# Kernel optimization log

Hardware: AMD Instinct MI355X
Metric: run time of the kernel (lower is better)

The kernel has to match this reference:

```python
import jax, jax.numpy as jnp
import numpy as np

# SAWB clip coefficients (statistics-aware weight binning): alpha = C1*sqrt(E[w^2]) + C2*E[|w|]
SAWB_C1 = 12.68
SAWB_C2 = -12.80
Q_LEVELS = 127.0  # symmetric 8-bit


def sawb_quantize_sparse(W, mask):
    """Quantize only the nonzero (masked) weight values per-tensor, SAWB clip.
    Returns dequantized sparse weight (zeros stay zero), matching the
    original module which stores nnz values + indices and quantizes the
    nnz value vector."""
    m = mask.astype(W.dtype)
    n = jnp.maximum(jnp.sum(m), 1.0)
    m1 = jnp.sum(jnp.abs(W) * m) / n          # E[|w|] over nonzeros
    m2 = jnp.sum((W * W) * m) / n             # E[w^2] over nonzeros
    alpha = SAWB_C1 * jnp.sqrt(m2) + SAWB_C2 * m1
    scale = alpha / Q_LEVELS
    q = jnp.round(jnp.clip(W / scale, -Q_LEVELS, Q_LEVELS))
    return (q * scale) * m


def setup_inputs() -> dict:
    key = jax.random.key(0)
    k1, k2, k3, k4 = jax.random.split(key, 4)
    B, IC, H, Wsp = 16, 64, 224, 224
    OC, K = 64, 3
    x = jax.random.normal(k1, (B, IC, H, Wsp), dtype=jnp.float32)
    W = jax.random.normal(k2, (OC, IC, K, K), dtype=jnp.float32) * 0.05
    mask = jax.random.uniform(k3, (OC, IC, K, K)) > 0.9
    bias = jax.random.normal(k4, (OC,), dtype=jnp.float32) * 0.01
    return {"x": x, "W": W, "mask": mask, "bias": bias}


def reference(x, W, mask, bias):
    # Dequantized sparse weight (equivalent math to gather-based sparse
    # quantized conv kernel with fused dequant)
    Wq = sawb_quantize_sparse(W, mask)
    y = jax.lax.conv_general_dilated(
        x, Wq,
        window_strides=(1, 1),
        padding=((1, 1), (1, 1)),
        dimension_numbers=("NCHW", "OIHW", "NCHW"),
    )
    return y + bias[None, :, None, None]
```

## Files before the change

### kernel.cpp

```cpp
#include <hip/hip_runtime.h>
#include <hip/hip_bf16.h>
#include <math.h>

typedef __bf16 bfx8 __attribute__((ext_vector_type(8)));
typedef float f32x4 __attribute__((ext_vector_type(4)));

#define NELEM_W 36864
#define CHW     50176

__device__ __forceinline__ int detect_mask_kind(const void* mask, int tid, int nthreads,
                                                int* s_flags, int* s_kind) {
  if (tid < 8) s_flags[tid] = 0;
  __syncthreads();
  const unsigned int* mw = (const unsigned int*)mask;
  int lowbf = 0, notf32 = 0, anyf32 = 0, noti32 = 0, anyi1 = 0;
  for (int i = tid; i < 1024; i += nthreads) {
    unsigned v = mw[i];
    if ((v & 0xFFFFu) == 0x3F80u) lowbf = 1;
    if (!(v == 0u || v == 0x3F800000u)) notf32 = 1;
    if (v == 0x3F800000u) anyf32 = 1;
    if (!(v == 0u || v == 1u)) noti32 = 1;
    if (v == 1u) anyi1 = 1;
  }
  if (lowbf)  atomicOr(&s_flags[0], 1);
  if (notf32) atomicOr(&s_flags[1], 1);
  if (anyf32) atomicOr(&s_flags[2], 1);
  if (noti32) atomicOr(&s_flags[3], 1);
  if (anyi1)  atomicOr(&s_flags[4], 1);
  __syncthreads();
  if (tid == 0) {
    int kind;
    if (s_flags[0]) kind = 3;
    else if (!s_flags[1] && s_flags[2]) kind = 2;
    else if (!s_flags[3] && s_flags[4]) kind = 1;
    else kind = 0;
    *s_kind = kind;
  }
  __syncthreads();
  return *s_kind;
}

__device__ __forceinline__ bool mask_val(const void* mask, int kind, int e) {
  switch (kind) {
    case 1:  return ((const int*)mask)[e] != 0;
    case 2:  return ((const float*)mask)[e] != 0.0f;
    case 3:  return ((const unsigned short*)mask)[e] != 0;
    default: return ((const unsigned char*)mask)[e] != 0;
  }
}

__global__ __launch_bounds__(512) void stats_kernel(const float* __restrict__ W,
                                                    const void* __restrict__ mask,
                                                    float* __restrict__ ws_part) {
  __shared__ int s_flags[8]; __shared__ int s_kind;
  __shared__ float s_red[3][8];
  const int tid = threadIdx.x;
  int kind = detect_mask_kind(mask, tid, 512, s_flags, &s_kind);
  int e = blockIdx.x * 512 + tid;
  float w = W[e];
  bool m = mask_val(mask, kind, e);
  float s1 = m ? fabsf(w) : 0.f;
  float s2 = m ? w * w   : 0.f;
  float c  = m ? 1.f     : 0.f;
  #pragma unroll
  for (int o = 32; o > 0; o >>= 1) {
    s1 += __shfl_down(s1, o); s2 += __shfl_down(s2, o); c += __shfl_down(c, o);
  }
  int wv = tid >> 6;
  if ((tid & 63) == 0) { s_red[0][wv] = s1; s_red[1][wv] = s2; s_red[2][wv] = c; }
  __syncthreads();
  if (tid == 0) {
    float a = 0, b = 0, cc = 0;
    for (int i = 0; i < 8; i++) { a += s_red[0][i]; b += s_red[1][i]; cc += s_red[2][i]; }
    ws_part[blockIdx.x * 4 + 0] = a;
    ws_part[blockIdx.x * 4 + 1] = b;
    ws_part[blockIdx.x * 4 + 2] = cc;
  }
}

__global__ __launch_bounds__(512) void quant_kernel(const float* __restrict__ W,
                                                    const void* __restrict__ mask,
                                                    const float* __restrict__ ws_part,
                                                    float* __restrict__ ws_scale,
                                                    unsigned short* __restrict__ Bq) {
  __shared__ int s_flags[8]; __shared__ int s_kind;
  __shared__ float s_scale;
  const int tid = threadIdx.x;
  int kind = detect_mask_kind(mask, tid, 512, s_flags, &s_kind);
  if (tid == 0) {
    float a = 0, b = 0, cc = 0;
    for (int i = 0; i < 72; i++) { a += ws_part[i*4]; b += ws_part[i*4+1]; cc += ws_part[i*4+2]; }
    float n  = fmaxf(cc, 1.f);
    float m1 = a / n, m2 = b / n;
    float alpha = 12.68f * sqrtf(m2) - 12.80f * m1;
    float scale = alpha / 127.0f;
    s_scale = scale;
    if (blockIdx.x == 0) ws_scale[0] = scale;
  }
  __syncthreads();
  float scale = s_scale;
  int e = blockIdx.x * 512 + tid;
  float w = W[e];
  float q = 0.f;
  if (mask_val(mask, kind, e)) {
    float v = w / scale;
    v = fminf(fmaxf(v, -127.f), 127.f);
    q = rintf(v);
  }
  int kxy = e % 9; int t = e / 9; int ic = t & 63; int oc = t >> 6;
  __bf16 qb = (__bf16)q;
  Bq[(kxy * 64 + oc) * 64 + ic] = *(unsigned short*)&qb;
}

__global__ __launch_bounds__(512, 6) void conv_kernel(const float* __restrict__ x,
    const unsigned short* __restrict__ Bq, const float* __restrict__ ws_scale,
    const float* __restrict__ bias, float* __restrict__ out)
{
  __shared__ __align__(16) unsigned char smem[6 * 66 * 128];
  const int tid = threadIdx.x;

  int lin = blockIdx.x + (int)(gridDim.x * (blockIdx.y + gridDim.y * blockIdx.z));
  int logical = (lin & 7) * 448 + (lin >> 3);
  const int bx = logical & 3;
  int rr = logical >> 2;
  const int by = rr % 56;
  const int b  = rr / 56;
  const int x0 = bx * 64;
  const int y0 = by * 4;

  for (int e = tid; e < 6 * 8 * 66; e += 512) {
    int col = e % 66; int t = e / 66; int icg = t & 7; int row = t >> 3;
    int grow = y0 - 1 + row, gcol = x0 - 1 + col;
    bfx8 v;
    if ((unsigned)grow < 224u && (unsigned)gcol < 224u) {
      const float* src = x + (((size_t)(b * 64 + icg * 8)) * 224 + grow) * 224 + gcol;
      #pragma unroll
      for (int j = 0; j < 8; j++) v[j] = (__bf16)src[j * CHW];
    } else {
      #pragma unroll
      for (int j = 0; j < 8; j++) v[j] = (__bf16)0.f;
    }
    int off = ((row * 66 + col) * 128 + icg * 16) ^ ((col & 7) << 4);
    *(bfx8*)(smem + off) = v;
  }
  __syncthreads();

  const int w = tid >> 6, lane = tid & 63;
  const int l15 = lane & 15, lg = lane >> 4;
  const int wrow = w >> 1;
  const int oc0  = (w & 1) * 32;

  f32x4 acc[4][2];
  #pragma unroll
  for (int m = 0; m < 4; m++) { acc[m][0] = {0.f,0.f,0.f,0.f}; acc[m][1] = {0.f,0.f,0.f,0.f}; }

  #pragma unroll
  for (int ky = 0; ky < 3; ky++) {
    const int lrow = wrow + ky;
    #pragma unroll
    for (int kx = 0; kx < 3; kx++) {
      #pragma unroll
      for (int icb = 0; icb < 2; icb++) {
        const int ick = icb * 32 + lg * 8;
        const unsigned short* wp = Bq + (((ky*3 + kx) * 64 + oc0 + l15) * 64 + ick);
        bfx8 wf0 = *(const bfx8*)wp;
        bfx8 wf1 = *(const bfx8*)(wp + 16 * 64);
        #pragma unroll
        for (int m = 0; m < 4; m++) {
          int colw = kx + m * 16 + l15;
          int off  = ((lrow * 66 + colw) * 128 + ick * 2) ^ ((colw & 7) << 4);
          bfx8 xf  = *(const bfx8*)(smem + off);
          acc[m][0] = __builtin_amdgcn_mfma_f32_16x16x32_bf16(wf0, xf, acc[m][0], 0, 0, 0);
          acc[m][1] = __builtin_amdgcn_mfma_f32_16x16x32_bf16(wf1, xf, acc[m][1], 0, 0, 0);
        }
      }
    }
  }

  const float scale = ws_scale[0];
  const int yr = y0 + wrow;
  #pragma unroll
  for (int m = 0; m < 4; m++) {
    const int gcol = x0 + m * 16 + l15;
    if (gcol < 224) {
      #pragma unroll
      for (int n = 0; n < 2; n++) {
        #pragma unroll
        for (int r = 0; r < 4; r++) {
          int oc = oc0 + n * 16 + lg * 4 + r;
          out[(((size_t)(b * 64 + oc)) * 224 + yr) * 224 + gcol] = acc[m][n][r] * scale + bias[oc];
        }
      }
    }
  }
}

extern "C" void kernel_launch(void* const* d_in, const int* in_sizes, int n_in,
                              void* d_out, int out_size, void* d_ws, size_t ws_size,
                              hipStream_t stream) {
  const float* x    = (const float*)d_in[0];
  const float* W    = (const float*)d_in[1];
  const void*  mask = d_in[2];
  const float* bias = (const float*)d_in[3];
  float* out = (float*)d_out;

  float*          ws_part  = (float*)d_ws;
  float*          ws_scale = (float*)((char*)d_ws + 2048);
  unsigned short* Bq       = (unsigned short*)((char*)d_ws + 4096);

  stats_kernel<<<72, 512, 0, stream>>>(W, mask, ws_part);
  quant_kernel<<<72, 512, 0, stream>>>(W, mask, ws_part, ws_scale, Bq);
  dim3 grid(4, 56, 16);
  conv_kernel<<<grid, 512, 0, stream>>>(x, Bq, ws_scale, bias, out);
}
```

Measured before the change: 475.9 us.

## Prepack input to padded bf16 channel-last layout and use async LDS loads with 32x32 MFMA

Adds a prepass kernel that converts the fp32 NCHW input into a padded, swizzled bf16 channel-interleaved buffer in workspace. The conv kernel then fills its LDS halo tile with direct global-to-LDS async 16-byte copies instead of strided fp32 gathers and conversions. It also switches to 32x32x16 MFMA tiles. This costs an extra full pass over the input (read fp32, write bf16) plus a workspace size check with a fallback path.

```diff
diff --git a/kernel.cpp b/kernel.cpp
--- a/kernel.cpp
+++ b/kernel.cpp
@@ -4,9 +4,22 @@
 
 typedef __bf16 bfx8 __attribute__((ext_vector_type(8)));
 typedef float f32x4 __attribute__((ext_vector_type(4)));
+typedef float f32x16 __attribute__((ext_vector_type(16)));
+typedef unsigned short u16x8 __attribute__((ext_vector_type(8)));
 
 #define NELEM_W 36864
 #define CHW     50176
+#define XB_ROWPITCH 28928
+#define XB_BYTES (16*224*XB_ROWPITCH)
+#define ZP_OFF   81920
+#define XB_OFF   98304
+#define WS_NEED  ((size_t)XB_OFF + (size_t)XB_BYTES)
+
+__device__ __forceinline__ void async_cp16(const void* g, void* l) {
+  __builtin_amdgcn_global_load_lds(
+      (const __attribute__((address_space(1))) unsigned int*)g,
+      (__attribute__((address_space(3))) unsigned int*)l, 16, 0, 0);
+}
 
 __device__ __forceinline__ int detect_mask_kind(const void* mask, int tid, int nthreads,
                                                 int* s_flags, int* s_kind) {
@@ -82,7 +95,8 @@
                                                     const void* __restrict__ mask,
                                                     const float* __restrict__ ws_part,
                                                     float* __restrict__ ws_scale,
-                                                    unsigned short* __restrict__ Bq) {
+                                                    unsigned short* __restrict__ Bq,
+                                                    char* __restrict__ zp) {
   __shared__ int s_flags[8]; __shared__ int s_kind;
   __shared__ float s_scale;
   const int tid = threadIdx.x;
@@ -100,21 +114,64 @@
   __syncthreads();
   float scale = s_scale;
   int e = blockIdx.x * 512 + tid;
-  float w = W[e];
-  float q = 0.f;
-  if (mask_val(mask, kind, e)) {
-    float v = w / scale;
-    v = fminf(fmaxf(v, -127.f), 127.f);
-    q = rintf(v);
-  }
-  int kxy = e % 9; int t = e / 9; int ic = t & 63; int oc = t >> 6;
-  __bf16 qb = (__bf16)q;
-  Bq[(kxy * 64 + oc) * 64 + ic] = *(unsigned short*)&qb;
-}
-
-__global__ __launch_bounds__(512, 6) void conv_kernel(const float* __restrict__ x,
-    const unsigned short* __restrict__ Bq, const float* __restrict__ ws_scale,
-    const float* __restrict__ bias, float* __restrict__ out)
+  if (e < NELEM_W) {
+    float w = W[e];
+    float q = 0.f;
+    if (mask_val(mask, kind, e)) {
+      float v = w / scale;
+      v = fminf(fmaxf(v, -127.f), 127.f);
+      q = rintf(v);
+    }
+    int kxy = e % 9; int t = e / 9; int ic = t & 63; int oc = t >> 6;
+    __bf16 qb = (__bf16)q;
+    Bq[(kxy * 64 + oc) * 64 + ic] = *(unsigned short*)&qb;
+  } else {
+    f32x4 z = {0.f, 0.f, 0.f, 0.f};
+    for (int u = tid; u < 528; u += 512) *(f32x4*)(zp + u * 16) = z;
+  }
+}
+
+__global__ __launch_bounds__(256) void prepass_kernel(const float* __restrict__ x,
+                                                      char* __restrict__ xb) {
+  __shared__ unsigned short lt[64][65];
+  const int cg = blockIdx.x;
+  const int h  = blockIdx.y;
+  const int b  = blockIdx.z;
+  const int t  = threadIdx.x;
+  const int c0 = cg * 64;
+  const int ncols = (226 - c0) < 64 ? (226 - c0) : 64;
+
+  {
+    int colt = t & 63, icq = t >> 6;
+    if (colt < ncols) {
+      int gcol = c0 + colt - 1;
+      bool valid = (unsigned)gcol < 224u;
+      const float* src = x + ((size_t)(b * 64 + icq * 16) * 224 + h) * 224 + gcol;
+      #pragma unroll
+      for (int j = 0; j < 16; j++) {
+        float v = valid ? src[(size_t)j * CHW] : 0.f;
+        __bf16 bv = (__bf16)v;
+        lt[icq * 16 + j][colt] = *(unsigned short*)&bv;
+      }
+    }
+  }
+  __syncthreads();
+  size_t rowbase = ((size_t)(b * 224 + h)) * XB_ROWPITCH;
+  for (int u = t; u < ncols * 8; u += 256) {
+    int colt = u >> 3, icg = u & 7;
+    int c = c0 + colt;
+    u16x8 v;
+    #pragma unroll
+    for (int j = 0; j < 8; j++) v[j] = lt[icg * 8 + j][colt];
+    int off = (c * 128 + icg * 16) ^ ((c & 7) << 4);
+    *(u16x8*)(xb + rowbase + off) = v;
+  }
+}
+
+__global__ __launch_bounds__(512, 6) void conv_kernel(const char* __restrict__ xb,
+    const char* __restrict__ zp, const unsigned short* __restrict__ Bq,
+    const float* __restrict__ ws_scale, const float* __restrict__ bias,
+    float* __restrict__ out)
 {
   __shared__ __align__(16) unsigned char smem[6 * 66 * 128];
   const int tid = threadIdx.x;
@@ -128,6 +185,86 @@
   const int x0 = bx * 64;
   const int y0 = by * 4;
 
+  const int w = tid >> 6, lane = tid & 63;
+
+  {
+    const size_t winoff = (size_t)x0 * 128;
+    #pragma unroll
+    for (int j = w; j < 48; j += 8) {
+      int row = j >> 3, chunk = j & 7;
+      int grow = y0 - 1 + row;
+      const char* src = ((unsigned)grow < 224u)
+          ? xb + ((size_t)(b * 224 + grow)) * XB_ROWPITCH + winoff + chunk * 1024
+          : zp + chunk * 1024;
+      async_cp16(src + lane * 16, smem + row * 8448 + chunk * 1024);
+    }
+    if (tid < 96) {
+      int row = tid >> 4, u = tid & 15;
+      int grow = y0 - 1 + row;
+      const char* src = ((unsigned)grow < 224u)
+          ? xb + ((size_t)(b * 224 + grow)) * XB_ROWPITCH + winoff + 8192 + u * 16
+          : zp + 8192 + u * 16;
+      *(f32x4*)(smem + row * 8448 + 8192 + u * 16) = *(const f32x4*)src;
+    }
+  }
+  __syncthreads();
+
+  const int wrow = w >> 1;
+  const int ch   = w & 1;
+  const int l31  = lane & 31, lg2 = lane >> 5;
+
+  f32x16 acc0 = {}, acc1 = {};
+
+  #pragma unroll
+  for (int ky = 0; ky < 3; ky++) {
+    const int lrow = wrow + ky;
+    #pragma unroll
+    for (int kx = 0; kx < 3; kx++) {
+      const int kxy = ky * 3 + kx;
+      #pragma unroll
+      for (int icq = 0; icq < 4; icq++) {
+        const int ick = icq * 16 + lg2 * 8;
+        const int ct  = kx + ch * 32 + l31;
+        const int off = (lrow * 66 + ct) * 128 + ((ick * 2) ^ ((ct & 7) << 4));
+        bfx8 xf = *(const bfx8*)(smem + off);
+        const unsigned short* wp = Bq + ((kxy * 64 + l31) * 64 + ick);
+        bfx8 wf0 = *(const bfx8*)wp;
+        bfx8 wf1 = *(const bfx8*)(wp + 32 * 64);
+        acc0 = __builtin_amdgcn_mfma_f32_32x32x16_bf16(wf0, xf, acc0, 0, 0, 0);
+        acc1 = __builtin_amdgcn_mfma_f32_32x32x16_bf16(wf1, xf, acc1, 0, 0, 0);
+      }
+    }
+  }
+
+  const float scale = ws_scale[0];
+  const int yr = y0 + wrow;
+  const int gcol = x0 + ch * 32 + l31;
+  if (gcol < 224) {
+    #pragma unroll
+    for (int r = 0; r < 16; r++) {
+      int ocr = (r & 3) + 8 * (r >> 2) + 4 * lg2;
+      size_t o0 = (((size_t)(b * 64 + ocr)) * 224 + yr) * 224 + gcol;
+      out[o0]              = acc0[r] * scale + bias[ocr];
+      out[o0 + 32 * CHW]   = acc1[r] * scale + bias[ocr + 32];
+    }
+  }
+}
+
+__global__ __launch_bounds__(512, 6) void conv_fallback(const float* __restrict__ x,
+    const unsigned short* __restrict__ Bq, const float* __restrict__ ws_scale,
+    const float* __restrict__ bias, float* __restrict__ out)
+{
+  __shared__ __align__(16) unsigned char smem[6 * 66 * 128];
+  const int tid = threadIdx.x;
+  int lin = blockIdx.x + (int)(gridDim.x * (blockIdx.y + gridDim.y * blockIdx.z));
+  int logical = (lin & 7) * 448 + (lin >> 3);
+  const int bx = logical & 3;
+  int rr = logical >> 2;
+  const int by = rr % 56;
+  const int b  = rr / 56;
+  const int x0 = bx * 64;
+  const int y0 = by * 4;
+
   for (int e = tid; e < 6 * 8 * 66; e += 512) {
     int col = e % 66; int t = e / 66; int icg = t & 7; int row = t >> 3;
     int grow = y0 - 1 + row, gcol = x0 - 1 + col;
@@ -153,7 +290,6 @@
   f32x4 acc[4][2];
   #pragma unroll
   for (int m = 0; m < 4; m++) { acc[m][0] = {0.f,0.f,0.f,0.f}; acc[m][1] = {0.f,0.f,0.f,0.f}; }
-
   #pragma unroll
   for (int ky = 0; ky < 3; ky++) {
     const int lrow = wrow + ky;
@@ -176,7 +312,6 @@
       }
     }
   }
-
   const float scale = ws_scale[0];
   const int yr = y0 + wrow;
   #pragma unroll
@@ -207,9 +342,18 @@
   float*          ws_part  = (float*)d_ws;
   float*          ws_scale = (float*)((char*)d_ws + 2048);
   unsigned short* Bq       = (unsigned short*)((char*)d_ws + 4096);
+  char*           zp       = (char*)d_ws + ZP_OFF;
+  char*           xb       = (char*)d_ws + XB_OFF;
 
   stats_kernel<<<72, 512, 0, stream>>>(W, mask, ws_part);
-  quant_kernel<<<72, 512, 0, stream>>>(W, mask, ws_part, ws_scale, Bq);
-  dim3 grid(4, 56, 16);
-  conv_kernel<<<grid, 512, 0, stream>>>(x, Bq, ws_scale, bias, out);
-}
+  quant_kernel<<<73, 512, 0, stream>>>(W, mask, ws_part, ws_scale, Bq, zp);
+
+  dim3 cgrid(4, 56, 16);
+  if (ws_size >= WS_NEED) {
+    dim3 pgrid(4, 224, 16);
+    prepass_kernel<<<pgrid, 256, 0, stream>>>(x, xb);
+    conv_kernel<<<cgrid, 512, 0, stream>>>(xb, zp, Bq, ws_scale, bias, out);
+  } else {
+    conv_fallback<<<cgrid, 512, 0, stream>>>(x, Bq, ws_scale, bias, out);
+  }
+}
```

New measurement: 613.4 us. 28.9% more time.
